# Optimization experiments

Hardware: AMD Instinct MI355X
Metric: run time of the kernel (lower is better)

## Reference

```python
import math
import jax, jax.numpy as jnp
import numpy as np

B, N, W, D, H = 16, 64, 128, 128, 4

def posenc(L, d):
    pos = jnp.arange(L, dtype=jnp.float32)[:, None]
    div = jnp.exp(jnp.arange(0, d, 2, dtype=jnp.float32) * (-math.log(10000.0) / d))
    pe = jnp.zeros((L, d), jnp.float32)
    pe = pe.at[:, 0::2].set(jnp.sin(pos * div))
    pe = pe.at[:, 1::2].set(jnp.cos(pos * div))
    return pe

def ln(x):
    # torch nn.LayerNorm(x.shape[1:]) created fresh each call: normalize over all non-batch dims, no affine
    ax = tuple(range(1, x.ndim))
    m = x.mean(ax, keepdims=True)
    v = ((x - m) ** 2).mean(ax, keepdims=True)
    return (x - m) / jnp.sqrt(v + 1e-5)

def conv1d(x, w, b):
    # x [B,C,L], w [Cout,Cin,K] (torch layout), VALID padding
    y = jax.lax.conv_general_dilated(x, w, (1,), 'VALID', dimension_numbers=('NCH', 'OIH', 'NCH'))
    return y + b[None, :, None]

def convt1d(x, w, b, stride, pad):
    # torch ConvTranspose1d, w [Cin,Cout,K]
    K = w.shape[2]
    w_ = jnp.flip(w, 2).transpose(1, 0, 2)  # [Cout,Cin,K]
    y = jax.lax.conv_general_dilated(x, w_, (1,), [(K - 1 - pad, K - 1 - pad)],
                                     lhs_dilation=(stride,), dimension_numbers=('NCH', 'OIH', 'NCH'))
    return y + b[None, :, None]

def mha(q, k, v, wi, bi, wo, bo):
    # torch nn.MultiheadAttention(batch_first=True), H heads
    d = q.shape[-1]
    qp = q @ wi[:d].T + bi[:d]
    kp = k @ wi[d:2 * d].T + bi[d:2 * d]
    vp = v @ wi[2 * d:].T + bi[2 * d:]
    def heads(t):
        b_, l_, _ = t.shape
        return t.reshape(b_, l_, H, d // H).transpose(0, 2, 1, 3)
    qh, kh, vh = heads(qp), heads(kp), heads(vp)
    s = jnp.einsum('bhqd,bhkd->bhqk', qh, kh) / jnp.sqrt(jnp.asarray(d // H, qh.dtype))
    o = jnp.einsum('bhqk,bhkd->bhqd', jax.nn.softmax(s, -1), vh)
    b_, l_ = q.shape[0], q.shape[1]
    return o.transpose(0, 2, 1, 3).reshape(b_, l_, d) @ wo.T + bo


def setup_inputs():
    key = jax.random.key(0)
    ks = iter(jax.random.split(key, 64))
    def w(shape, s=0.05):
        return jax.random.normal(next(ks), shape, jnp.float32) * s
    inp = {}
    inp['tokens'] = jax.random.randint(next(ks), (B, N, W), 0, 257, jnp.int32)
    inp['emb_table'] = w((257, D), 1.0)
    for nm in ['ce', 'ct', 'cg', 'ces', 'cts']:
        inp['w_' + nm] = w((D, D, 3))
        inp['b_' + nm] = w((D,))
    inp['mha_wi'] = w((3 * D, D)); inp['mha_bi'] = w((3 * D,))
    inp['mha_wo'] = w((D, D)); inp['mha_bo'] = w((D,))
    s = 1.0 / math.sqrt(D)
    inp['tgt1'] = jax.random.uniform(next(ks), (1, D), jnp.float32, -s, s)
    inp['tgt2'] = jax.random.uniform(next(ks), (1, D), jnp.float32, -s, s)
    for nm in ['mu', 'lv', 'di']:
        inp['w_' + nm] = w((D, D)); inp['b_' + nm] = w((D,))
    inp['eps'] = jax.random.normal(next(ks), (B, D), jnp.float32)
    inp['dk_w'] = w((32, 32)); inp['dk_b'] = w((32,))
    inp['dv_w'] = w((32, 32)); inp['dv_b'] = w((32,))
    inp['wt1'] = w((32, 64, 3)); inp['bt1'] = w((64,))
    inp['wt2'] = w((64, 128, 3)); inp['bt2'] = w((128,))
    for nm in ['sq', 'sk', 'sv']:
        inp[nm + '_w'] = w((128, 128)); inp[nm + '_b'] = w((128,))
    inp['wt3'] = w((128, 128, 3)); inp['bt3'] = w((128,))
    return inp


def reference(tokens, emb_table, w_ce, b_ce, w_ct, b_ct, w_cg, b_cg, w_ces, b_ces, w_cts, b_cts,
              mha_wi, mha_bi, mha_wo, mha_bo, tgt1, tgt2,
              w_mu, b_mu, w_lv, b_lv, w_di, b_di, eps,
              dk_w, dk_b, dv_w, dv_b, wt1, bt1, wt2, bt2,
              sq_w, sq_b, sk_w, sk_b, sv_w, sv_b, wt3, bt3):
    emb = emb_table[tokens] + posenc(W, D)                    # [B,N,W,D]
    flat = emb.reshape(B * N, W, D)                           # batch the per-sample torch loop

    def word_branch(wc, bc, act):
        h = act(conv1d(flat.transpose(0, 2, 1), wc, bc)).transpose(0, 2, 1)  # [BN,W-2,D]
        return mha(h, h, h, mha_wi, mha_bi, mha_wo, mha_bo)

    a_e = jax.nn.elu(word_branch(w_ce, b_ce, jax.nn.elu))
    a_t = jnp.tanh(word_branch(w_ct, b_ct, jnp.tanh))
    xw = ln((a_e * a_t).reshape(B, N, W - 2, D)).reshape(B * N, W - 2, D)

    h = jax.nn.elu(conv1d(xw.transpose(0, 2, 1), w_cg, b_cg)).transpose(0, 2, 1)  # [BN,W-4,D]
    q1 = jnp.broadcast_to(tgt1[None], (B * N, 1, D))
    out = mha(q1, h, h, mha_wi, mha_bi, mha_wo, mha_bo)[:, 0, :].reshape(B, N, D)

    se = out + posenc(N, D)                                   # sentence level

    def sent_branch(wc, bc, act):
        hh = act(conv1d(se.transpose(0, 2, 1), wc, bc)).transpose(0, 2, 1)       # [B,N-2,D]
        return mha(hh, hh, hh, mha_wi, mha_bi, mha_wo, mha_bo)

    s_e = jax.nn.elu(sent_branch(w_ces, b_ces, jax.nn.elu))
    s_t = jnp.tanh(sent_branch(w_cts, b_cts, jnp.tanh))
    xs = ln(s_e * s_t)
    q2 = jnp.broadcast_to(tgt2[None], (B, 1, D))
    doc = mha(q2, xs, xs, mha_wi, mha_bi, mha_wo, mha_bo)[:, 0, :]

    mu = doc @ w_mu.T + b_mu
    lv = doc @ w_lv.T + b_lv
    z = mu + eps * jnp.exp(0.5 * lv)

    h = (z @ w_di.T + b_di).reshape(B, 32, -1)                # [B,32,4]
    L = h.shape[2]
    k = jnp.einsum('oi,bil->bol', dk_w, h) + dk_b[None, :, None]
    v = jnp.einsum('oi,bil->bol', dv_w, h) + dv_b[None, :, None]
    kh = k.reshape(B, H, 8, L)
    vh = v.reshape(B, H, 8, L)
    att = jax.nn.softmax(jnp.einsum('bhdl,bhdm->bhlm', kh, vh) / jnp.sqrt(8.0), -1)
    h = jax.nn.elu(jnp.einsum('bhlm,bhdm->bhld', att, vh).reshape(B, 32, L))
    h = jax.nn.elu(ln(convt1d(h, wt1, bt1, 2, 1)))            # [B,64,7]
    h = jax.nn.elu(ln(convt1d(h, wt2, bt2, 2, 1)))            # [B,128,13]
    L2 = h.shape[2]
    qc = jnp.einsum('oi,bil->bol', sq_w, h) + sq_b[None, :, None]
    kc = jnp.einsum('oi,bil->bol', sk_w, h) + sk_b[None, :, None]
    vc = jnp.einsum('oi,bil->bol', sv_w, h) + sv_b[None, :, None]
    qh = qc.reshape(B, H, 32, L2)
    khh = kc.reshape(B, H, 32, L2)
    att = jax.nn.softmax(jnp.einsum('bhdl,bhdm->bhlm', qh, khh) / jnp.sqrt(32.0), -1)
    vr = vc.reshape(B, H, 32, L2).reshape(B, H, L2, 32)       # faithful torch .view reinterpretation
    h = jax.nn.elu(jnp.einsum('bhlm,bhmd->bhld', att, vr).reshape(B, 128, L2))
    recon = jax.nn.sigmoid(ln(convt1d(h, wt3, bt3, 1, 1)))    # [B,128,13]
    return recon, mu, lv
```

## Files before the change

### kernel.cpp

```cpp
#include <hip/hip_runtime.h>
#include <hip/hip_bf16.h>

typedef __hip_bfloat16 bf16;
typedef __attribute__((ext_vector_type(8))) short bf16x8;
typedef __attribute__((ext_vector_type(4))) float f32x4;

__device__ __forceinline__ float b2f(bf16 x){ return __bfloat162float(x); }
__device__ __forceinline__ bf16  f2b(float x){ return __float2bfloat16(x); }
__device__ __forceinline__ unsigned short b2u(bf16 x){ union{bf16 b; unsigned short u;} c; c.b = x; return c.u; }

#define LOG2E 1.4426950408889634f
#define QSC (0.17677669529663687f * LOG2E)

__device__ __forceinline__ float fexp2(float x){
  float r; asm("v_exp_f32 %0, %1" : "=v"(r) : "v"(x)); return r;
}
__device__ __forceinline__ float fast_exp(float x){ return fexp2(x * LOG2E); }
__device__ __forceinline__ float eluf(float x){ return x > 0.f ? x : fast_exp(x) - 1.f; }
__device__ __forceinline__ float fast_tanh(float x){
  float cx = fminf(fmaxf(x, -15.f), 15.f);
  float t = fexp2(cx * (2.f*LOG2E));
  return (t - 1.f) / (t + 1.f);
}

#define PE_C (-0.07195578415606394f)

__device__ __forceinline__ float pe_val(int pos, int d){
  int j2 = d & ~1;
  float ang = (float)pos * expf((float)j2 * PE_C);
  return (d & 1) ? cosf(ang) : sinf(ang);
}

__device__ __forceinline__ void pack_one(const float* __restrict__ W, bf16* __restrict__ out,
                                         int K, int N, int conv, int qscale, int t){
  int j = t & 7, lane = (t >> 3) & 63;
  int rest = t >> 9; int NT = N >> 4;
  int nt = rest % NT; int kb = rest / NT;
  int k = kb*32 + ((lane >> 4) << 3) + j;
  int n = nt*16 + (lane & 15);
  float v = conv ? W[n*384 + (k & 127)*3 + (k >> 7)] : W[(long)n*K + k];
  if (qscale && n < 128) v *= QSC;
  out[t] = f2b(v);
}

__global__ void k_prep(const float* __restrict__ w_ce, const float* __restrict__ w_ct,
                       const float* __restrict__ w_cg, const float* __restrict__ w_ces,
                       const float* __restrict__ w_cts, const float* __restrict__ wi,
                       const float* __restrict__ wo,
                       bf16* P_CE, bf16* P_CT, bf16* P_CG, bf16* P_CES, bf16* P_CTS,
                       bf16* P_WI, bf16* P_WO, float* __restrict__ pet){
  int bid = blockIdx.x;
  if (bid < 1152){
    int grp = bid / 192; int t = (bid % 192)*256 + threadIdx.x;
    const float* W; bf16* out; int K, N, conv, qs = 0;
    if      (grp == 0){ W = w_ce;  out = P_CE;  K=384; N=128; conv=1; }
    else if (grp == 1){ W = w_ct;  out = P_CT;  K=384; N=128; conv=1; }
    else if (grp == 2){ W = w_cg;  out = P_CG;  K=384; N=128; conv=1; }
    else if (grp == 3){ W = w_ces; out = P_CES; K=384; N=128; conv=1; }
    else if (grp == 4){ W = w_cts; out = P_CTS; K=384; N=128; conv=1; }
    else              { W = wi;    out = P_WI;  K=128; N=384; conv=0; qs=1; }
    pack_one(W, out, K, N, conv, qs, t);
  } else if (bid < 1216){
    int t = (bid - 1152)*256 + threadIdx.x;
    pack_one(wo, P_WO, 128, 128, 0, 0, t);
  } else {
    int i = (bid - 1216)*256 + threadIdx.x;
    if (i < 16384) pet[i] = pe_val(i >> 7, i & 127);
  }
}

__global__ void k_qprep(const float* __restrict__ wi, const float* __restrict__ bi,
                        const float* __restrict__ t1, const float* __restrict__ t2,
                        float* __restrict__ rkv){
  int tid = threadIdx.x;
  __shared__ float qps[256];
  {
    int which = tid >> 7, jj = tid & 127;
    const float* t = which ? t2 : t1;
    float a = bi[jj];
    for (int i = 0; i < 128; ++i) a += wi[jj*128 + i] * t[i];
    qps[tid] = a;
  }
  __syncthreads();
  int i = tid & 127, which = tid >> 7;
  for (int h = 0; h < 4; ++h){
    float a = 0.f;
    for (int d = 0; d < 32; ++d) a += qps[which*128 + h*32 + d] * wi[(128 + h*32 + d)*128 + i];
    rkv[which*512 + h*128 + i] = a;
  }
}

__global__ void k_embed8(const int* __restrict__ tok, const float* __restrict__ tab,
                         const float* __restrict__ pet, bf16* __restrict__ out){
  int t = blockIdx.x*256 + threadIdx.x;
  int q = t & 15;
  int flat = t >> 4; int w = flat & 127;
  int tk = tok[flat];
  const float* ta = tab + tk*128 + q*8;
  const float* pe = pet + (w << 7) + q*8;
  bf16 ob[8];
  #pragma unroll
  for (int i = 0; i < 8; ++i) ob[i] = f2b(ta[i] + pe[i]);
  *(f32x4*)(out + (size_t)t*8) = *(f32x4*)ob;
}

__global__ void k_se(const bf16* __restrict__ in, const float* __restrict__ pet, bf16* __restrict__ out){
  int idx = blockIdx.x*256 + threadIdx.x;
  int d = idx & 127; int n = (idx >> 7) & 63;
  out[idx] = f2b(b2f(in[idx]) + pet[(n << 7) + d]);
}

__global__ __launch_bounds__(256)
void k_gemm_mfma(const bf16* __restrict__ A, const bf16* __restrict__ Bp_, const bf16* __restrict__ Bp2,
                 const float* __restrict__ bias_, const float* __restrict__ bias2,
                 bf16* __restrict__ C_, bf16* __restrict__ C2p,
                 const bf16* __restrict__ mul,
                 int M, int K, int a_lout, int a_lind, int lda,
                 int NT, int n0t, int ldc, int act_, int act2,
                 const float* __restrict__ lnst, int lngrp){
  const bf16* Bp = Bp_; const float* bias = bias_; bf16* C = C_; int act = act_;
  if (blockIdx.z){ Bp = Bp2; bias = bias2; C = C2p; act = act2; }

  __shared__ f32x4 AsV[2][512];
  char* As0 = (char*)AsV[0];
  char* As1 = (char*)AsV[1];
  int tid = threadIdx.x;
  int lane = tid & 63, wave = tid >> 6;
  int wm = wave >> 1, wn = wave & 1;
  int m0 = blockIdx.x*128;
  int by = blockIdx.y;

  long offA[2]; bool okA[2]; float lnm[2], lnr[2]; int sbyte[2];
  #pragma unroll
  for (int p = 0; p < 2; ++p){
    int e = tid + p*256;
    int row = e >> 2, kq = e & 3, m = m0 + row;
    okA[p] = (m < M);
    long off = 0;
    if (okA[p]){
      off = (a_lout > 0) ? (long)(m / a_lout)*a_lind + (long)(m % a_lout)*128 + kq*8
                         : (long)m*lda + kq*8;
    }
    offA[p] = off;
    lnm[p] = 0.f; lnr[p] = 1.f;
    if (lnst && okA[p]){ int g = (int)(off / (long)lngrp); lnm[p] = lnst[2*g]; lnr[p] = lnst[2*g+1]; }
    sbyte[p] = (row*64 + kq*16) ^ ((row & 7) << 4);
  }
  auto loadA = [&](int p, int kb)->float4{
    float4 v = make_float4(0.f,0.f,0.f,0.f);
    if (okA[p]){
      v = *(const float4*)(A + offA[p] + kb*32);
      if (lnst){
        bf16* pp = (bf16*)&v; bf16 oo[8];
        #pragma unroll
        for (int u = 0; u < 8; ++u) oo[u] = f2b((b2f(pp[u]) - lnm[p]) * lnr[p]);
        v = *(float4*)&oo[0];
      }
    }
    return v;
  };

  const bf16* bptr[4];
  size_t bstep = (size_t)NT*512;
  #pragma unroll
  for (int fn = 0; fn < 4; ++fn){
    int ntile = n0t + by*8 + wn*4 + fn;
    bptr[fn] = Bp + ((size_t)ntile*64 + lane)*8;
  }
  int abyte[4];
  #pragma unroll
  for (int fm = 0; fm < 4; ++fm){
    int row = wm*64 + fm*16 + (lane & 15);
    abyte[fm] = (row*64 + ((lane >> 4) << 4)) ^ ((row & 7) << 4);
  }

  f32x4 acc[4][4];
  #pragma unroll
  for (int i = 0; i < 4; ++i)
    #pragma unroll
    for (int j = 0; j < 4; ++j) acc[i][j] = (f32x4){0.f,0.f,0.f,0.f};

  float4 va0 = loadA(0, 0), va1 = loadA(1, 0);
  *(float4*)(As0 + sbyte[0]) = va0;
  *(float4*)(As0 + sbyte[1]) = va1;
  __syncthreads();

  int nk = K >> 5;
  for (int kb = 0; kb < nk; ++kb){
    char* cur = (kb & 1) ? As1 : As0;
    char* nxt = (kb & 1) ? As0 : As1;
    bool more = (kb + 1) < nk;
    if (more){ va0 = loadA(0, kb+1); va1 = loadA(1, kb+1); }
    bf16x8 bfr[4];
    #pragma unroll
    for (int fn = 0; fn < 4; ++fn) bfr[fn] = *(const bf16x8*)(bptr[fn] + (size_t)kb*bstep);
    bf16x8 afr[4];
    #pragma unroll
    for (int fm = 0; fm < 4; ++fm) afr[fm] = *(const bf16x8*)(cur + abyte[fm]);
    #pragma unroll
    for (int fm = 0; fm < 4; ++fm)
      #pragma unroll
      for (int fn = 0; fn < 4; ++fn)
        acc[fm][fn] = __builtin_amdgcn_mfma_f32_16x16x32_bf16(afr[fm], bfr[fn], acc[fm][fn], 0, 0, 0);
    if (more){
      *(float4*)(nxt + sbyte[0]) = va0;
      *(float4*)(nxt + sbyte[1]) = va1;
    }
    __syncthreads();
  }

  #pragma unroll
  for (int fm = 0; fm < 4; ++fm){
    #pragma unroll
    for (int r = 0; r < 4; ++r){
      int m = m0 + wm*64 + fm*16 + ((lane >> 4) << 2) + r;
      if (m >= M) continue;
      #pragma unroll
      for (int fn = 0; fn < 4; ++fn){
        int n = by*128 + wn*64 + fn*16 + (lane & 15);
        float v = acc[fm][fn][r] + (bias ? bias[n] : 0.f);
        if (act == 1) v = eluf(v);
        else if (act == 2) v = fast_tanh(v);
        if (mul) v *= b2f(mul[(long)m*ldc + n]);
        C[(long)m*ldc + n] = f2b(v);
      }
    }
  }
}

template<int L>
__global__ __launch_bounds__(256)
void k_attn_fused(const bf16* __restrict__ X, const bf16* __restrict__ Pwi,
                  const float* __restrict__ bi, bf16* __restrict__ o){
  constexpr int KB  = (L + 31) / 32;
  constexpr int MT  = KB * 2;
  constexpr int WMT = MT / 4;
  constexpr int NP  = KB * 32;
  constexpr int PRS = NP * 2;

  __shared__ alignas(16) char As[NP*256];
  __shared__ alignas(16) char Qb[NP*64];
  __shared__ alignas(16) char Kb[NP*64];
  __shared__ alignas(16) char Vt[32*PRS];
  char* Pb = As;

  int tid = threadIdx.x;
  int s = blockIdx.x >> 2, h = blockIdx.x & 3;
  const bf16* xb = X + (size_t)s*L*128;

  for (int e = tid; e < NP*16; e += 256){
    int row = e >> 4, c = e & 15;
    float4 v = make_float4(0.f,0.f,0.f,0.f);
    if (row < L) v = *(const float4*)(xb + (size_t)row*128 + c*8);
    *(float4*)(As + ((row*256 + c*16) ^ ((row & 7) << 4))) = v;
  }
  __syncthreads();

  int lane = tid & 63, wave = tid >> 6;
  int col = lane & 15;

  __builtin_amdgcn_s_setprio(1);
  #pragma unroll
  for (int mt = 0; mt < WMT; ++mt){
    int mtile = wave*WMT + mt;
    int arow = mtile*16 + col;
    bf16x8 a4[4];
    #pragma unroll
    for (int kb = 0; kb < 4; ++kb)
      a4[kb] = *(const bf16x8*)(As + ((arow*256 + kb*64 + ((lane >> 4) << 4)) ^ ((arow & 7) << 4)));
    #pragma unroll
    for (int which = 0; which < 3; ++which){
      f32x4 av[2];
      #pragma unroll
      for (int nt = 0; nt < 2; ++nt){
        int ntile = which*8 + h*2 + nt;
        float bia = bi[which*128 + h*32 + nt*16 + col];
        if (which == 0) bia *= QSC;
        av[nt] = (f32x4){bia, bia, bia, bia};
        #pragma unroll
        for (int kb = 0; kb < 4; ++kb){
          bf16x8 bfr = *(const bf16x8*)(Pwi + (((size_t)kb*24 + ntile)*64 + lane)*8);
          av[nt] = __builtin_amdgcn_mfma_f32_16x16x32_bf16(a4[kb], bfr, av[nt], 0, 0, 0);
        }
      }
      #pragma unroll
      for (int r = 0; r < 4; ++r){
        int row = mtile*16 + ((lane >> 4) << 2) + r;
        if (which < 2){
          unsigned pk = (unsigned)b2u(f2b(av[0][r])) | ((unsigned)b2u(f2b(av[1][r])) << 16);
          char* dst = which ? Kb : Qb;
          *(unsigned*)(dst + ((row*64 + col*4) ^ ((row & 7) << 4))) = pk;
        } else {
          int pos = (row & 15)*MT + (row >> 4);
          #pragma unroll
          for (int nt = 0; nt < 2; ++nt){
            int d = nt*16 + col;
            *(bf16*)(Vt + ((d*PRS + pos*2) ^ ((d & 7) << 4))) = f2b(av[nt][r]);
          }
        }
      }
    }
  }
  __builtin_amdgcn_s_setprio(0);
  __syncthreads();

  f32x4 acc[WMT][MT];
  #pragma unroll
  for (int mt = 0; mt < WMT; ++mt)
    #pragma unroll
    for (int nt = 0; nt < MT; ++nt) acc[mt][nt] = (f32x4){0.f,0.f,0.f,0.f};

  bf16x8 af[WMT];
  #pragma unroll
  for (int mt = 0; mt < WMT; ++mt){
    int row = (wave*WMT + mt)*16 + col;
    af[mt] = *(const bf16x8*)(Qb + ((row*64 + ((lane >> 4) << 4)) ^ ((row & 7) << 4)));
  }
  __builtin_amdgcn_s_setprio(1);
  #pragma unroll
  for (int nt = 0; nt < MT; ++nt){
    int rk2 = nt*16 + col;
    bf16x8 bfk = *(const bf16x8*)(Kb + ((rk2*64 + ((lane >> 4) << 4)) ^ ((rk2 & 7) << 4)));
    #pragma unroll
    for (int mt = 0; mt < WMT; ++mt)
      acc[mt][nt] = __builtin_amdgcn_mfma_f32_16x16x32_bf16(af[mt], bfk, acc[mt][nt], 0, 0, 0);
  }
  __builtin_amdgcn_s_setprio(0);

  const bool lastMask = col >= (L - (MT-1)*16);
  float pinv[WMT][4];
  #pragma unroll
  for (int mt = 0; mt < WMT; ++mt){
    #pragma unroll
    for (int r = 0; r < 4; ++r){
      float mx = -1e30f;
      #pragma unroll
      for (int nt = 0; nt < MT; ++nt){
        float v = acc[mt][nt][r];
        if (nt == MT-1 && lastMask){ v = -1e30f; acc[mt][nt][r] = v; }
        mx = fmaxf(mx, v);
      }
      mx = fmaxf(mx, __shfl_xor(mx, 1));
      mx = fmaxf(mx, __shfl_xor(mx, 2));
      mx = fmaxf(mx, __shfl_xor(mx, 4));
      mx = fmaxf(mx, __shfl_xor(mx, 8));
      float sum = 0.f;
      bf16 prow[MT];
      #pragma unroll
      for (int nt = 0; nt < MT; ++nt){
        float p = fexp2(acc[mt][nt][r] - mx);
        prow[nt] = f2b(p);
        sum += p;
      }
      sum += __shfl_xor(sum, 1);
      sum += __shfl_xor(sum, 2);
      sum += __shfl_xor(sum, 4);
      sum += __shfl_xor(sum, 8);
      pinv[mt][r] = 1.f / sum;
      int row = (wave*WMT + mt)*16 + ((lane >> 4) << 2) + r;
      char* dst = Pb + ((row*PRS + col*(MT*2)) ^ ((row & 7) << 4));
      if constexpr (MT == 8) *(f32x4*)dst = *(f32x4*)prow;
      else                   *(float2*)dst = *(float2*)prow;
    }
  }

  #pragma unroll
  for (int mt = 0; mt < WMT; ++mt){
    int mtile = wave*WMT + mt;
    f32x4 o0 = (f32x4){0.f,0.f,0.f,0.f}, o1 = (f32x4){0.f,0.f,0.f,0.f};
    __builtin_amdgcn_s_setprio(1);
    #pragma unroll
    for (int kb = 0; kb < KB; ++kb){
      int row = mtile*16 + col;
      bf16x8 pa = *(const bf16x8*)(Pb + ((row*PRS + kb*64 + ((lane >> 4) << 4)) ^ ((row & 7) << 4)));
      int d0 = col;
      bf16x8 v0 = *(const bf16x8*)(Vt + ((d0*PRS + kb*64 + ((lane >> 4) << 4)) ^ ((d0 & 7) << 4)));
      bf16x8 v1 = *(const bf16x8*)(Vt + (((d0+16)*PRS + kb*64 + ((lane >> 4) << 4)) ^ (((d0+16) & 7) << 4)));
      o0 = __builtin_amdgcn_mfma_f32_16x16x32_bf16(pa, v0, o0, 0, 0, 0);
      o1 = __builtin_amdgcn_mfma_f32_16x16x32_bf16(pa, v1, o1, 0, 0, 0);
    }
    __builtin_amdgcn_s_setprio(0);
    #pragma unroll
    for (int r = 0; r < 4; ++r){
      int row = mtile*16 + ((lane >> 4) << 2) + r;
      if (row < L){
        size_t ob = ((size_t)s*L + row)*128 + h*32 + col;
        o[ob]      = f2b(o0[r] * pinv[mt][r]);
        o[ob + 16] = f2b(o1[r] * pinv[mt][r]);
      }
    }
  }
}

template<int L>
__global__ __launch_bounds__(256)
void k_attn_tgt(const bf16* __restrict__ hin, const float* __restrict__ rk,
                const float* __restrict__ wi, const float* __restrict__ bi,
                bf16* __restrict__ outp){
  __shared__ alignas(16) char Hs[L*256];
  __shared__ float RKs[512];
  __shared__ float Ps[512];
  __shared__ float Cs[512];
  int tid = threadIdx.x, lane = tid & 63, wave = tid >> 6;
  int s = blockIdx.x;
  const bf16* hb = hin + (size_t)s*L*128;
  for (int e = tid; e < L*16; e += 256){
    int row = e >> 4, c = e & 15;
    *(float4*)(Hs + row*256 + ((c ^ (row & 7)) << 4)) = *(const float4*)(hb + row*128 + c*8);
  }
  for (int e = tid; e < 512; e += 256) RKs[e] = rk[e];
  __syncthreads();

  int j0 = lane, j1 = lane + 64;
  float v0 = -1e30f, v1 = -1e30f;
  if (j0 < L){
    float a = 0.f;
    #pragma unroll
    for (int c = 0; c < 16; ++c){
      bf16x8 x = *(const bf16x8*)(Hs + j0*256 + ((c ^ (j0 & 7)) << 4));
      #pragma unroll
      for (int u = 0; u < 8; ++u) a += b2f(((bf16*)&x)[u]) * RKs[wave*128 + c*8 + u];
    }
    v0 = a * 0.17677669529663687f;
  }
  if (j1 < L){
    float a = 0.f;
    #pragma unroll
    for (int c = 0; c < 16; ++c){
      bf16x8 x = *(const bf16x8*)(Hs + j1*256 + ((c ^ (j1 & 7)) << 4));
      #pragma unroll
      for (int u = 0; u < 8; ++u) a += b2f(((bf16*)&x)[u]) * RKs[wave*128 + c*8 + u];
    }
    v1 = a * 0.17677669529663687f;
  }
  float mx = fmaxf(v0, v1);
  #pragma unroll
  for (int off = 32; off; off >>= 1) mx = fmaxf(mx, __shfl_xor(mx, off));
  float e0 = (j0 < L) ? fast_exp(v0 - mx) : 0.f;
  float e1 = (j1 < L) ? fast_exp(v1 - mx) : 0.f;
  float sum = e0 + e1;
  #pragma unroll
  for (int off = 32; off; off >>= 1) sum += __shfl_xor(sum, off);
  float inv = 1.f / sum;
  Ps[wave*128 + j0] = e0 * inv;
  Ps[wave*128 + j1] = e1 * inv;

  int i0 = lane*2;
  float c0 = 0.f, c1 = 0.f;
  for (int j = 0; j < L; ++j){
    float p = Ps[wave*128 + j];
    short2 w2 = *(const short2*)(Hs + j*256 + (((i0 >> 3) ^ (j & 7)) << 4) + (i0 & 7)*2);
    c0 += p * b2f(*(bf16*)&w2.x);
    c1 += p * b2f(*(bf16*)&w2.y);
  }
  Cs[wave*128 + i0]     = c0;
  Cs[wave*128 + i0 + 1] = c1;
  __syncthreads();

  if (tid < 128){
    int h2 = tid >> 5;
    float a = bi[256 + tid];
    const float* wr = wi + (size_t)(256 + tid)*128;
    for (int i = 0; i < 128; ++i) a += wr[i] * Cs[h2*128 + i];
    outp[(size_t)s*128 + tid] = f2b(a);
  }
}

__global__ void k_ln_partial(const bf16* __restrict__ x, float* __restrict__ part, int GS, int P){
  int pi = blockIdx.x % P;
  int chunk8 = GS / P / 8;
  size_t base = (size_t)(blockIdx.x / P)*GS + (size_t)pi*(GS/P);
  float s = 0.f, s2 = 0.f;
  for (int i = threadIdx.x; i < chunk8; i += 256){
    f32x4 raw = *(const f32x4*)(x + base + (size_t)i*8);
    const bf16* xb = (const bf16*)&raw;
    #pragma unroll
    for (int j = 0; j < 8; ++j){ float v = b2f(xb[j]); s += v; s2 += v*v; }
  }
  #pragma unroll
  for (int off = 32; off; off >>= 1){ s += __shfl_xor(s, off); s2 += __shfl_xor(s2, off); }
  __shared__ float sh[8];
  int lane = threadIdx.x & 63, wv = threadIdx.x >> 6;
  if (lane == 0){ sh[wv] = s; sh[4 + wv] = s2; }
  __syncthreads();
  if (threadIdx.x == 0){
    part[blockIdx.x*2]     = sh[0]+sh[1]+sh[2]+sh[3];
    part[blockIdx.x*2 + 1] = sh[4]+sh[5]+sh[6]+sh[7];
  }
}

__global__ void k_ln_fin(const float* __restrict__ part, float* __restrict__ stats, int P, int GS){
  int g = blockIdx.x;
  float s = 0.f, s2 = 0.f;
  for (int i = threadIdx.x; i < P; i += 256){ s += part[(g*P + i)*2]; s2 += part[(g*P + i)*2 + 1]; }
  #pragma unroll
  for (int off = 32; off; off >>= 1){ s += __shfl_xor(s, off); s2 += __shfl_xor(s2, off); }
  __shared__ float sh[8];
  int lane = threadIdx.x & 63, wv = threadIdx.x >> 6;
  if (lane == 0){ sh[wv] = s; sh[4 + wv] = s2; }
  __syncthreads();
  if (threadIdx.x == 0){
    float S = sh[0]+sh[1]+sh[2]+sh[3], S2 = sh[4]+sh[5]+sh[6]+sh[7];
    float mean = S / GS;
    float var = S2 / GS - mean*mean;
    stats[g*2] = mean; stats[g*2 + 1] = rsqrtf(var + 1e-5f);
  }
}

__global__ void k_ln_small_bf16(const bf16* __restrict__ x, bf16* __restrict__ y, int n){
  int g = blockIdx.x;
  const bf16* xb = x + (size_t)g*n;
  bf16* yb = y + (size_t)g*n;
  float s = 0.f, s2 = 0.f;
  for (int i = threadIdx.x; i < n; i += 256){ float v = b2f(xb[i]); s += v; s2 += v*v; }
  #pragma unroll
  for (int off = 32; off; off >>= 1){ s += __shfl_xor(s, off); s2 += __shfl_xor(s2, off); }
  __shared__ float sh[8];  __shared__ float ms[2];
  int lane = threadIdx.x & 63, wv = threadIdx.x >> 6;
  if (lane == 0){ sh[wv] = s; sh[4 + wv] = s2; }
  __syncthreads();
  if (threadIdx.x == 0){
    float S = sh[0]+sh[1]+sh[2]+sh[3], S2 = sh[4]+sh[5]+sh[6]+sh[7];
    float mean = S / n;
    ms[0] = mean; ms[1] = rsqrtf(S2 / n - mean*mean + 1e-5f);
  }
  __syncthreads();
  float mean = ms[0], inv = ms[1];
  for (int i = threadIdx.x; i < n; i += 256) yb[i] = f2b((b2f(xb[i]) - mean)*inv);
}

__global__ __launch_bounds__(256)
void k_decoder(const bf16* __restrict__ DOC,
               const float* __restrict__ w_mu, const float* __restrict__ b_mu,
               const float* __restrict__ w_lv, const float* __restrict__ b_lv,
               const float* __restrict__ eps,
               const float* __restrict__ w_di, const float* __restrict__ b_di,
               const float* __restrict__ dk_w, const float* __restrict__ dk_b,
               const float* __restrict__ dv_w, const float* __restrict__ dv_b,
               const float* __restrict__ wt1, const float* __restrict__ bt1,
               const float* __restrict__ wt2, const float* __restrict__ bt2,
               const float* __restrict__ sq_w, const float* __restrict__ sq_b,
               const float* __restrict__ sk_w, const float* __restrict__ sk_b,
               const float* __restrict__ sv_w, const float* __restrict__ sv_b,
               const float* __restrict__ wt3, const float* __restrict__ bt3,
               float* __restrict__ dout){
  int b = blockIdx.x, tid = threadIdx.x;
  __shared__ float Zs[128], H3[128], KD[128], VD[128], D1[128];
  __shared__ float C1[448], D2[448];
  __shared__ float C2a[1664], D3[1664];
  __shared__ float QC[1664], KC[1664], VC[1664], D4[1664], C3a[1664];
  __shared__ float sc[676];
  __shared__ float red[8], ms[2];

  auto lnact = [&](const float* x, float* y, int n, int act){
    float s = 0.f, s2 = 0.f;
    for (int i = tid; i < n; i += 256){ float v = x[i]; s += v; s2 += v*v; }
    #pragma unroll
    for (int o = 32; o; o >>= 1){ s += __shfl_xor(s, o); s2 += __shfl_xor(s2, o); }
    int lane = tid & 63, wv = tid >> 6;
    if (lane == 0){ red[wv] = s; red[4+wv] = s2; }
    __syncthreads();
    if (tid == 0){
      float S = red[0]+red[1]+red[2]+red[3], S2 = red[4]+red[5]+red[6]+red[7];
      float mean = S/n; ms[0] = mean; ms[1] = rsqrtf(S2/n - mean*mean + 1e-5f);
    }
    __syncthreads();
    float mean = ms[0], inv = ms[1];
    for (int i = tid; i < n; i += 256){
      float v = (x[i]-mean)*inv;
      if (act == 1) v = eluf(v);
      else if (act == 3) v = 1.f/(1.f + fast_exp(-v));
      y[i] = v;
    }
    __syncthreads();
  };

  if (tid < 128){
    const bf16* dr = DOC + b*128;
    float mu = b_mu[tid], lv = b_lv[tid];
    for (int i = 0; i < 128; ++i){
      float x = b2f(dr[i]);
      mu += x * w_mu[tid*128 + i];
      lv += x * w_lv[tid*128 + i];
    }
    dout[26624 + b*128 + tid] = mu;
    dout[28672 + b*128 + tid] = lv;
    Zs[tid] = mu + eps[b*128 + tid] * fast_exp(0.5f*lv);
  }
  __syncthreads();
  if (tid < 128){
    float a = b_di[tid];
    for (int i = 0; i < 128; ++i) a += Zs[i] * w_di[tid*128 + i];
    H3[tid] = a;
  }
  __syncthreads();
  if (tid < 128){
    int l = tid & 3, o2 = tid >> 2;
    float ak = dk_b[o2], av = dv_b[o2];
    for (int i = 0; i < 32; ++i){
      float xv = H3[i*4 + l];
      ak += dk_w[o2*32 + i]*xv;
      av += dv_w[o2*32 + i]*xv;
    }
    KD[tid] = ak; VD[tid] = av;
  }
  __syncthreads();
  if (tid < 64){
    int h = tid >> 4, l = (tid >> 2) & 3, m = tid & 3;
    float a = 0.f;
    #pragma unroll
    for (int d = 0; d < 8; ++d) a += KD[(h*8+d)*4 + l] * VD[(h*8+d)*4 + m];
    sc[tid] = a * 0.35355339059327373f;
  }
  __syncthreads();
  if (tid < 16){
    int base = tid*4;
    float mx = fmaxf(fmaxf(sc[base],sc[base+1]),fmaxf(sc[base+2],sc[base+3]));
    float e0=fast_exp(sc[base]-mx), e1=fast_exp(sc[base+1]-mx), e2=fast_exp(sc[base+2]-mx), e3=fast_exp(sc[base+3]-mx);
    float inv = 1.f/(e0+e1+e2+e3);
    sc[base]=e0*inv; sc[base+1]=e1*inv; sc[base+2]=e2*inv; sc[base+3]=e3*inv;
  }
  __syncthreads();
  if (tid < 128){
    int h = tid >> 5, rem = tid & 31, l = rem >> 3, d = rem & 7;
    float a = 0.f;
    #pragma unroll
    for (int m = 0; m < 4; ++m) a += sc[h*16 + l*4 + m] * VD[(h*8+d)*4 + m];
    D1[tid] = eluf(a);
  }
  __syncthreads();
  for (int idx = tid; idx < 448; idx += 256){
    int co = idx / 7, lo = idx % 7;
    float a = bt1[co];
    for (int k = 0; k < 3; ++k){
      int t = lo + 1 - k;
      if (t < 0 || (t & 1)) continue;
      int li = t >> 1; if (li >= 4) continue;
      float aa = 0.f;
      for (int ci = 0; ci < 32; ++ci) aa += D1[ci*4 + li] * wt1[ci*192 + co*3 + k];
      a += aa;
    }
    C1[idx] = a;
  }
  __syncthreads();
  lnact(C1, D2, 448, 1);
  for (int idx = tid; idx < 1664; idx += 256){
    int co = idx / 13, lo = idx % 13;
    float a = bt2[co];
    for (int k = 0; k < 3; ++k){
      int t = lo + 1 - k;
      if (t < 0 || (t & 1)) continue;
      int li = t >> 1; if (li >= 7) continue;
      float aa = 0.f;
      for (int ci = 0; ci < 64; ++ci) aa += D2[ci*7 + li] * wt2[ci*384 + co*3 + k];
      a += aa;
    }
    C2a[idx] = a;
  }
  __syncthreads();
  lnact(C2a, D3, 1664, 1);
  for (int idx = tid; idx < 1664; idx += 256){
    int o = idx / 13, l = idx % 13;
    float a1 = sq_b[o], a2 = sk_b[o], a3 = sv_b[o];
    for (int i = 0; i < 128; ++i){
      float xv = D3[i*13 + l];
      a1 += sq_w[o*128 + i]*xv;
      a2 += sk_w[o*128 + i]*xv;
      a3 += sv_w[o*128 + i]*xv;
    }
    QC[idx] = a1; KC[idx] = a2; VC[idx] = a3;
  }
  __syncthreads();
  for (int idx = tid; idx < 676; idx += 256){
    int h = idx / 169, rem = idx % 169;
    int l = rem / 13, m = rem % 13;
    float a = 0.f;
    #pragma unroll
    for (int d = 0; d < 32; ++d) a += QC[h*416 + d*13 + l] * KC[h*416 + d*13 + m];
    sc[idx] = a * 0.17677669529663687f;
  }
  __syncthreads();
  if (tid < 52){
    int h = tid / 13, l = tid % 13;
    float* row = sc + h*169 + l*13;
    float mx = -1e30f;
    for (int m = 0; m < 13; ++m) mx = fmaxf(mx, row[m]);
    float ssum = 0.f;
    for (int m = 0; m < 13; ++m){ float p = fast_exp(row[m]-mx); row[m] = p; ssum += p; }
    float inv = 1.f/ssum;
    for (int m = 0; m < 13; ++m) row[m] *= inv;
  }
  __syncthreads();
  for (int idx = tid; idx < 1664; idx += 256){
    int h = idx / 416, rem = idx % 416;
    int l = rem >> 5, d = rem & 31;
    float a = 0.f;
    for (int m = 0; m < 13; ++m) a += sc[h*169 + l*13 + m] * VC[h*416 + m*32 + d];
    D4[idx] = eluf(a);
  }
  __syncthreads();
  for (int idx = tid; idx < 1664; idx += 256){
    int co = idx / 13, lo = idx % 13;
    float a = bt3[co];
    for (int k = 0; k < 3; ++k){
      int li = lo + 1 - k;
      if (li < 0 || li >= 13) continue;
      float aa = 0.f;
      for (int ci = 0; ci < 128; ++ci) aa += D4[ci*13 + li] * wt3[ci*384 + co*3 + k];
      a += aa;
    }
    C3a[idx] = a;
  }
  __syncthreads();
  lnact(C3a, D4, 1664, 3);
  for (int i = tid; i < 1664; i += 256) dout[b*1664 + i] = D4[i];
}

extern "C" void kernel_launch(void* const* d_in, const int* in_sizes, int n_in,
                              void* d_out, int out_size, void* d_ws, size_t ws_size,
                              hipStream_t stream){
  const int*   tokens = (const int*)  d_in[0];
  const float* tab    = (const float*)d_in[1];
  const float* w_ce = (const float*)d_in[2];  const float* b_ce = (const float*)d_in[3];
  const float* w_ct = (const float*)d_in[4];  const float* b_ct = (const float*)d_in[5];
  const float* w_cg = (const float*)d_in[6];  const float* b_cg = (const float*)d_in[7];
  const float* w_ces= (const float*)d_in[8];  const float* b_ces= (const float*)d_in[9];
  const float* w_cts= (const float*)d_in[10]; const float* b_cts= (const float*)d_in[11];
  const float* wi   = (const float*)d_in[12]; const float* bi   = (const float*)d_in[13];
  const float* wo   = (const float*)d_in[14]; const float* bo   = (const float*)d_in[15];
  const float* tgt1 = (const float*)d_in[16]; const float* tgt2 = (const float*)d_in[17];
  const float* w_mu = (const float*)d_in[18]; const float* b_mu = (const float*)d_in[19];
  const float* w_lv = (const float*)d_in[20]; const float* b_lv = (const float*)d_in[21];
  const float* w_di = (const float*)d_in[22]; const float* b_di = (const float*)d_in[23];
  const float* epsb = (const float*)d_in[24];
  const float* dk_w = (const float*)d_in[25]; const float* dk_b = (const float*)d_in[26];
  const float* dv_w = (const float*)d_in[27]; const float* dv_b = (const float*)d_in[28];
  const float* wt1  = (const float*)d_in[29]; const float* bt1  = (const float*)d_in[30];
  const float* wt2  = (const float*)d_in[31]; const float* bt2  = (const float*)d_in[32];
  const float* sq_w = (const float*)d_in[33]; const float* sq_b = (const float*)d_in[34];
  const float* sk_w = (const float*)d_in[35]; const float* sk_b = (const float*)d_in[36];
  const float* sv_w = (const float*)d_in[37]; const float* sv_b = (const float*)d_in[38];
  const float* wt3  = (const float*)d_in[39]; const float* bt3  = (const float*)d_in[40];

  float* dout = (float*)d_out;

  char* ws = (char*)d_ws;
  size_t off = 0;
  auto take = [&](size_t bytes)->char*{ char* p = ws + off; off += (bytes + 255) & ~(size_t)255; return p; };
  bf16* EMB  = (bf16*)take(16777216ull*2);
  bf16* HB   = (bf16*)take(16515072ull*2);
  bf16* OB   = (bf16*)take(16515072ull*2);
  bf16* AE   = (bf16*)take(16515072ull*2);
  bf16* O1   = (bf16*)take(131072ull*2);
  bf16* OUTB = (bf16*)take(131072ull*2);
  bf16* SEB  = (bf16*)take(131072ull*2);
  bf16* SH   = (bf16*)take(126976ull*2);
  bf16* SCT  = (bf16*)take(126976ull*2);
  bf16* SO   = (bf16*)take(126976ull*2);
  bf16* SAE  = (bf16*)take(126976ull*2);
  bf16* XS   = (bf16*)take(126976ull*2);
  bf16* DO1  = (bf16*)take(2048ull*2);
  bf16* DOC  = (bf16*)take(2048ull*2);
  float* RK  = (float*)take(1024*4);
  float* PART= (float*)take(2016ull*2*4);
  float* STATS=(float*)take(32*4);
  float* PET = (float*)take(16384*4);
  bf16* P_CE = (bf16*)take(49152ull*2);
  bf16* P_CT = (bf16*)take(49152ull*2);
  bf16* P_CG = (bf16*)take(49152ull*2);
  bf16* P_CES= (bf16*)take(49152ull*2);
  bf16* P_CTS= (bf16*)take(49152ull*2);
  bf16* P_WI = (bf16*)take(49152ull*2);
  bf16* P_WO = (bf16*)take(16384ull*2);
  (void)ws_size; (void)in_sizes; (void)n_in; (void)out_size;

  auto cdiv = [](long a, long b){ return (int)((a + b - 1)/b); };
  auto gemm = [&](const bf16* A, const bf16* Bpp, const float* bias, bf16* C, const bf16* mul,
                  int M, int N, int K, int a_lout, int a_lind, int lda, int NT, int n0t, int ldc, int act,
                  const float* lnst, int lngrp){
    dim3 g(cdiv(M,128), N/128, 1);
    k_gemm_mfma<<<g, 256, 0, stream>>>(A, Bpp, Bpp, bias, bias, C, C, mul,
                                       M, K, a_lout, a_lind, lda, NT, n0t, ldc, act, act, lnst, lngrp);
  };
  auto gemmz = [&](const bf16* A, const bf16* Bp1, const float* b1, bf16* C1, int act1,
                   const bf16* Bp2, const float* b2, bf16* C2, int act2,
                   int M, int N, int K, int a_lout, int a_lind, int lda, int NT, int n0t, int ldc){
    dim3 g(cdiv(M,128), N/128, 2);
    k_gemm_mfma<<<g, 256, 0, stream>>>(A, Bp1, Bp2, b1, b2, C1, C2, nullptr,
                                       M, K, a_lout, a_lind, lda, NT, n0t, ldc, act1, act2, nullptr, 0);
  };

  k_prep<<<1280, 256, 0, stream>>>(w_ce, w_ct, w_cg, w_ces, w_cts, wi, wo,
                                   P_CE, P_CT, P_CG, P_CES, P_CTS, P_WI, P_WO, PET);
  k_qprep<<<1, 256, 0, stream>>>(wi, bi, tgt1, tgt2, RK);
  k_embed8<<<8192, 256, 0, stream>>>(tokens, tab, PET, EMB);

  gemmz(EMB, P_CE, b_ce, HB, 1, P_CT, b_ct, OB, 2, 129024, 128, 384, 126, 16384, 0, 8, 0, 128);

  k_attn_fused<126><<<4096, 256, 0, stream>>>(HB, P_WI, bi, EMB);
  gemm(EMB, P_WO, bo, AE, nullptr, 129024, 128, 128, 0, 0, 128, 8, 0, 128, 1, nullptr, 0);

  k_attn_fused<126><<<4096, 256, 0, stream>>>(OB, P_WI, bi, EMB);
  gemm(EMB, P_WO, bo, HB, AE, 129024, 128, 128, 0, 0, 128, 8, 0, 128, 2, nullptr, 0);

  k_ln_partial<<<2016, 256, 0, stream>>>(HB, PART, 1032192, 126);
  k_ln_fin<<<16, 256, 0, stream>>>(PART, STATS, 126, 1032192);

  gemm(HB, P_CG, b_cg, OB, nullptr, 126976, 128, 384, 124, 16128, 0, 8, 0, 128, 1, STATS, 1032192);

  k_attn_tgt<124><<<1024, 256, 0, stream>>>(OB, RK, wi, bi, O1);
  gemm(O1, P_WO, bo, OUTB, nullptr, 1024, 128, 128, 0, 0, 128, 8, 0, 128, 0, nullptr, 0);

  k_se<<<512, 256, 0, stream>>>(OUTB, PET, SEB);

  gemmz(SEB, P_CES, b_ces, SH, 1, P_CTS, b_cts, SCT, 2, 992, 128, 384, 62, 8192, 0, 8, 0, 128);

  k_attn_fused<62><<<64, 256, 0, stream>>>(SH, P_WI, bi, SO);
  gemm(SO, P_WO, bo, SAE, nullptr, 992, 128, 128, 0, 0, 128, 8, 0, 128, 1, nullptr, 0);

  k_attn_fused<62><<<64, 256, 0, stream>>>(SCT, P_WI, bi, SO);
  gemm(SO, P_WO, bo, SH, SAE, 992, 128, 128, 0, 0, 128, 8, 0, 128, 2, nullptr, 0);

  k_ln_small_bf16<<<16, 256, 0, stream>>>(SH, XS, 7936);

  k_attn_tgt<62><<<16, 256, 0, stream>>>(XS, RK + 512, wi, bi, DO1);
  gemm(DO1, P_WO, bo, DOC, nullptr, 16, 128, 128, 0, 0, 128, 8, 0, 128, 0, nullptr, 0);

  k_decoder<<<16, 256, 0, stream>>>(DOC, w_mu, b_mu, w_lv, b_lv, epsb, w_di, b_di,
                                    dk_w, dk_b, dv_w, dv_b, wt1, bt1, wt2, bt2,
                                    sq_w, sq_b, sk_w, sk_b, sv_w, sv_b, wt3, bt3, dout);
}
```

Before: 701.4 us.

## Split monolithic decoder kernel into multi-block stages for more parallelism

The single 16-block decoder kernel is broken into several launches: an initial stage, transposed convolutions spread over 128 blocks, a per-element channel projection, per-head attention over 64 blocks, and separate layernorm kernels. The goal is to spread the serial decoder tail across more CUs instead of 16. In exchange, intermediates now round-trip through global memory and there are extra kernel launches.

```diff
diff --git a/kernel.cpp b/kernel.cpp
--- a/kernel.cpp
+++ b/kernel.cpp
@@ -529,51 +529,48 @@
   for (int i = threadIdx.x; i < n; i += 256) yb[i] = f2b((b2f(xb[i]) - mean)*inv);
 }
 
+__global__ void k_ln_small_f32(const float* __restrict__ x, float* __restrict__ y, int n, int act){
+  int g = blockIdx.x;
+  const float* xb = x + (size_t)g*n;
+  float* yb = y + (size_t)g*n;
+  float s = 0.f, s2 = 0.f;
+  for (int i = threadIdx.x; i < n; i += 256){ float v = xb[i]; s += v; s2 += v*v; }
+  #pragma unroll
+  for (int off = 32; off; off >>= 1){ s += __shfl_xor(s, off); s2 += __shfl_xor(s2, off); }
+  __shared__ float sh[8];  __shared__ float ms[2];
+  int lane = threadIdx.x & 63, wv = threadIdx.x >> 6;
+  if (lane == 0){ sh[wv] = s; sh[4 + wv] = s2; }
+  __syncthreads();
+  if (threadIdx.x == 0){
+    float S = sh[0]+sh[1]+sh[2]+sh[3], S2 = sh[4]+sh[5]+sh[6]+sh[7];
+    float mean = S / n;
+    ms[0] = mean; ms[1] = rsqrtf(S2 / n - mean*mean + 1e-5f);
+  }
+  __syncthreads();
+  float mean = ms[0], inv = ms[1];
+  for (int i = threadIdx.x; i < n; i += 256){
+    float v = (xb[i] - mean)*inv;
+    if (act == 1) v = eluf(v);
+    else if (act == 3) v = 1.f/(1.f + fast_exp(-v));
+    yb[i] = v;
+  }
+}
+
 __global__ __launch_bounds__(256)
-void k_decoder(const bf16* __restrict__ DOC,
-               const float* __restrict__ w_mu, const float* __restrict__ b_mu,
-               const float* __restrict__ w_lv, const float* __restrict__ b_lv,
-               const float* __restrict__ eps,
-               const float* __restrict__ w_di, const float* __restrict__ b_di,
-               const float* __restrict__ dk_w, const float* __restrict__ dk_b,
-               const float* __restrict__ dv_w, const float* __restrict__ dv_b,
-               const float* __restrict__ wt1, const float* __restrict__ bt1,
-               const float* __restrict__ wt2, const float* __restrict__ bt2,
-               const float* __restrict__ sq_w, const float* __restrict__ sq_b,
-               const float* __restrict__ sk_w, const float* __restrict__ sk_b,
-               const float* __restrict__ sv_w, const float* __restrict__ sv_b,
-               const float* __restrict__ wt3, const float* __restrict__ bt3,
-               float* __restrict__ dout){
+void k_dec_a(const bf16* __restrict__ DOC,
+             const float* __restrict__ w_mu, const float* __restrict__ b_mu,
+             const float* __restrict__ w_lv, const float* __restrict__ b_lv,
+             const float* __restrict__ eps,
+             const float* __restrict__ w_di, const float* __restrict__ b_di,
+             const float* __restrict__ dk_w, const float* __restrict__ dk_b,
+             const float* __restrict__ dv_w, const float* __restrict__ dv_b,
+             const float* __restrict__ wt1, const float* __restrict__ bt1,
+             float* __restrict__ dout, float* __restrict__ DEC2){
   int b = blockIdx.x, tid = threadIdx.x;
   __shared__ float Zs[128], H3[128], KD[128], VD[128], D1[128];
-  __shared__ float C1[448], D2[448];
-  __shared__ float C2a[1664], D3[1664];
-  __shared__ float QC[1664], KC[1664], VC[1664], D4[1664], C3a[1664];
-  __shared__ float sc[676];
+  __shared__ float C1[448];
+  __shared__ float sc[64];
   __shared__ float red[8], ms[2];
-
-  auto lnact = [&](const float* x, float* y, int n, int act){
-    float s = 0.f, s2 = 0.f;
-    for (int i = tid; i < n; i += 256){ float v = x[i]; s += v; s2 += v*v; }
-    #pragma unroll
-    for (int o = 32; o; o >>= 1){ s += __shfl_xor(s, o); s2 += __shfl_xor(s2, o); }
-    int lane = tid & 63, wv = tid >> 6;
-    if (lane == 0){ red[wv] = s; red[4+wv] = s2; }
-    __syncthreads();
-    if (tid == 0){
-      float S = red[0]+red[1]+red[2]+red[3], S2 = red[4]+red[5]+red[6]+red[7];
-      float mean = S/n; ms[0] = mean; ms[1] = rsqrtf(S2/n - mean*mean + 1e-5f);
-    }
-    __syncthreads();
-    float mean = ms[0], inv = ms[1];
-    for (int i = tid; i < n; i += 256){
-      float v = (x[i]-mean)*inv;
-      if (act == 1) v = eluf(v);
-      else if (act == 3) v = 1.f/(1.f + fast_exp(-v));
-      y[i] = v;
-    }
-    __syncthreads();
-  };
 
   if (tid < 128){
     const bf16* dr = DOC + b*128;
@@ -643,77 +640,102 @@
     C1[idx] = a;
   }
   __syncthreads();
-  lnact(C1, D2, 448, 1);
-  for (int idx = tid; idx < 1664; idx += 256){
-    int co = idx / 13, lo = idx % 13;
-    float a = bt2[co];
-    for (int k = 0; k < 3; ++k){
-      int t = lo + 1 - k;
-      if (t < 0 || (t & 1)) continue;
-      int li = t >> 1; if (li >= 7) continue;
-      float aa = 0.f;
-      for (int ci = 0; ci < 64; ++ci) aa += D2[ci*7 + li] * wt2[ci*384 + co*3 + k];
-      a += aa;
-    }
-    C2a[idx] = a;
-  }
-  __syncthreads();
-  lnact(C2a, D3, 1664, 1);
-  for (int idx = tid; idx < 1664; idx += 256){
-    int o = idx / 13, l = idx % 13;
-    float a1 = sq_b[o], a2 = sk_b[o], a3 = sv_b[o];
-    for (int i = 0; i < 128; ++i){
-      float xv = D3[i*13 + l];
-      a1 += sq_w[o*128 + i]*xv;
-      a2 += sk_w[o*128 + i]*xv;
-      a3 += sv_w[o*128 + i]*xv;
-    }
-    QC[idx] = a1; KC[idx] = a2; VC[idx] = a3;
-  }
-  __syncthreads();
-  for (int idx = tid; idx < 676; idx += 256){
-    int h = idx / 169, rem = idx % 169;
-    int l = rem / 13, m = rem % 13;
+  {
+    float s = 0.f, s2 = 0.f;
+    for (int i = tid; i < 448; i += 256){ float v = C1[i]; s += v; s2 += v*v; }
+    #pragma unroll
+    for (int o = 32; o; o >>= 1){ s += __shfl_xor(s, o); s2 += __shfl_xor(s2, o); }
+    int lane = tid & 63, wv = tid >> 6;
+    if (lane == 0){ red[wv] = s; red[4+wv] = s2; }
+    __syncthreads();
+    if (tid == 0){
+      float S = red[0]+red[1]+red[2]+red[3], S2 = red[4]+red[5]+red[6]+red[7];
+      float mean = S/448.f; ms[0] = mean; ms[1] = rsqrtf(S2/448.f - mean*mean + 1e-5f);
+    }
+    __syncthreads();
+    float mean = ms[0], inv = ms[1];
+    for (int i = tid; i < 448; i += 256)
+      DEC2[b*448 + i] = eluf((C1[i]-mean)*inv);
+  }
+}
+
+__global__ void k_chanproj3(const float* __restrict__ x,
+                            const float* __restrict__ w1, const float* __restrict__ b1,
+                            const float* __restrict__ w2, const float* __restrict__ b2,
+                            const float* __restrict__ w3, const float* __restrict__ b3,
+                            float* __restrict__ y1, float* __restrict__ y2, float* __restrict__ y3,
+                            int Bn, int C, int L){
+  int idx = blockIdx.x*256 + threadIdx.x;
+  if (idx >= Bn*C*L) return;
+  int l = idx % L; int t2 = idx / L; int o = t2 % C; int b = t2 / C;
+  float a1 = b1[o], a2 = b2[o], a3 = b3[o];
+  const float* xb = x + (size_t)b*C*L + l;
+  for (int i = 0; i < C; ++i){
+    float xv = xb[i*L];
+    a1 += w1[(size_t)o*C + i]*xv;
+    a2 += w2[(size_t)o*C + i]*xv;
+    a3 += w3[(size_t)o*C + i]*xv;
+  }
+  y1[idx] = a1; y2[idx] = a2; y3[idx] = a3;
+}
+
+__global__ __launch_bounds__(256)
+void k_dec_attn2(const float* __restrict__ qc, const float* __restrict__ kc,
+                 const float* __restrict__ vc, float* __restrict__ out){
+  int b = blockIdx.x >> 2, h = blockIdx.x & 3, tid = threadIdx.x;
+  __shared__ float sc[169];
+  const float* qb = qc + b*1664 + h*416;
+  const float* kb = kc + b*1664 + h*416;
+  const float* vb = vc + b*1664 + h*416;
+  if (tid < 169){
+    int l = tid/13, m = tid - l*13;
     float a = 0.f;
     #pragma unroll
-    for (int d = 0; d < 32; ++d) a += QC[h*416 + d*13 + l] * KC[h*416 + d*13 + m];
-    sc[idx] = a * 0.17677669529663687f;
-  }
-  __syncthreads();
-  if (tid < 52){
-    int h = tid / 13, l = tid % 13;
-    float* row = sc + h*169 + l*13;
+    for (int d = 0; d < 32; ++d) a += qb[d*13 + l] * kb[d*13 + m];
+    sc[tid] = a * 0.17677669529663687f;
+  }
+  __syncthreads();
+  if (tid < 13){
     float mx = -1e30f;
-    for (int m = 0; m < 13; ++m) mx = fmaxf(mx, row[m]);
-    float ssum = 0.f;
-    for (int m = 0; m < 13; ++m){ float p = fast_exp(row[m]-mx); row[m] = p; ssum += p; }
-    float inv = 1.f/ssum;
-    for (int m = 0; m < 13; ++m) row[m] *= inv;
-  }
-  __syncthreads();
-  for (int idx = tid; idx < 1664; idx += 256){
-    int h = idx / 416, rem = idx % 416;
-    int l = rem >> 5, d = rem & 31;
+    for (int m = 0; m < 13; ++m) mx = fmaxf(mx, sc[tid*13 + m]);
+    float s = 0.f;
+    for (int m = 0; m < 13; ++m){ float p = fast_exp(sc[tid*13 + m] - mx); sc[tid*13 + m] = p; s += p; }
+    float inv = 1.f/s;
+    for (int m = 0; m < 13; ++m) sc[tid*13 + m] *= inv;
+  }
+  __syncthreads();
+  for (int idx = tid; idx < 416; idx += 256){
+    int l = idx >> 5, d = idx & 31;
     float a = 0.f;
-    for (int m = 0; m < 13; ++m) a += sc[h*169 + l*13 + m] * VC[h*416 + m*32 + d];
-    D4[idx] = eluf(a);
-  }
-  __syncthreads();
-  for (int idx = tid; idx < 1664; idx += 256){
-    int co = idx / 13, lo = idx % 13;
-    float a = bt3[co];
-    for (int k = 0; k < 3; ++k){
-      int li = lo + 1 - k;
-      if (li < 0 || li >= 13) continue;
-      float aa = 0.f;
-      for (int ci = 0; ci < 128; ++ci) aa += D4[ci*13 + li] * wt3[ci*384 + co*3 + k];
-      a += aa;
-    }
-    C3a[idx] = a;
-  }
-  __syncthreads();
-  lnact(C3a, D4, 1664, 3);
-  for (int i = tid; i < 1664; i += 256) dout[b*1664 + i] = D4[i];
+    for (int m = 0; m < 13; ++m) a += sc[l*13 + m] * vb[m*32 + d];
+    out[b*1664 + h*416 + idx] = eluf(a);
+  }
+}
+
+__global__ __launch_bounds__(256)
+void k_convt(const float* __restrict__ x, const float* __restrict__ w,
+             const float* __restrict__ bias, float* __restrict__ y,
+             int Bn, int Ci, int Co, int Lin, int Lout, int stride, int pad, int nch){
+  __shared__ float xs[1664];
+  int b = blockIdx.x / nch;
+  int c0 = (blockIdx.x % nch)*16;
+  int tid = threadIdx.x;
+  for (int i = tid; i < Ci*Lin; i += 256) xs[i] = x[(size_t)b*Ci*Lin + i];
+  __syncthreads();
+  int co = c0 + (tid & 15);
+  int lo = tid >> 4;
+  if (co >= Co || lo >= Lout) return;
+  float a = bias[co];
+  for (int k = 0; k < 3; ++k){
+    int t = lo + pad - k;
+    if (t < 0 || (t % stride)) continue;
+    int li = t / stride;
+    if (li >= Lin) continue;
+    float aa = 0.f;
+    for (int ci = 0; ci < Ci; ++ci) aa += xs[ci*Lin + li] * w[(size_t)ci*Co*3 + co*3 + k];
+    a += aa;
+  }
+  y[(size_t)b*Co*Lout + co*Lout + lo] = a;
 }
 
 extern "C" void kernel_launch(void* const* d_in, const int* in_sizes, int n_in,
@@ -764,6 +786,14 @@
   float* RK  = (float*)take(1024*4);
   float* PART= (float*)take(2016ull*2*4);
   float* STATS=(float*)take(32*4);
+  float* DEC2= (float*)take(7168*4);
+  float* C2  = (float*)take(26624*4);
+  float* DEC3= (float*)take(26624*4);
+  float* QC  = (float*)take(26624*4);
+  float* KC  = (float*)take(26624*4);
+  float* VC  = (float*)take(26624*4);
+  float* DEC4= (float*)take(26624*4);
+  float* C3  = (float*)take(26624*4);
   float* PET = (float*)take(16384*4);
   bf16* P_CE = (bf16*)take(49152ull*2);
   bf16* P_CT = (bf16*)take(49152ull*2);
@@ -783,10 +813,10 @@
                                        M, K, a_lout, a_lind, lda, NT, n0t, ldc, act, act, lnst, lngrp);
   };
   auto gemmz = [&](const bf16* A, const bf16* Bp1, const float* b1, bf16* C1, int act1,
-                   const bf16* Bp2, const float* b2, bf16* C2, int act2,
+                   const bf16* Bp2, const float* b2, bf16* C2p, int act2,
                    int M, int N, int K, int a_lout, int a_lind, int lda, int NT, int n0t, int ldc){
     dim3 g(cdiv(M,128), N/128, 2);
-    k_gemm_mfma<<<g, 256, 0, stream>>>(A, Bp1, Bp2, b1, b2, C1, C2, nullptr,
+    k_gemm_mfma<<<g, 256, 0, stream>>>(A, Bp1, Bp2, b1, b2, C1, C2p, nullptr,
                                        M, K, a_lout, a_lind, lda, NT, n0t, ldc, act1, act2, nullptr, 0);
   };
 
@@ -826,7 +856,13 @@
   k_attn_tgt<62><<<16, 256, 0, stream>>>(XS, RK + 512, wi, bi, DO1);
   gemm(DO1, P_WO, bo, DOC, nullptr, 16, 128, 128, 0, 0, 128, 8, 0, 128, 0, nullptr, 0);
 
-  k_decoder<<<16, 256, 0, stream>>>(DOC, w_mu, b_mu, w_lv, b_lv, epsb, w_di, b_di,
-                                    dk_w, dk_b, dv_w, dv_b, wt1, bt1, wt2, bt2,
-                                    sq_w, sq_b, sk_w, sk_b, sv_w, sv_b, wt3, bt3, dout);
-}
+  k_dec_a<<<16, 256, 0, stream>>>(DOC, w_mu, b_mu, w_lv, b_lv, epsb, w_di, b_di,
+                                  dk_w, dk_b, dv_w, dv_b, wt1, bt1, dout, DEC2);
+  k_convt<<<16*8, 256, 0, stream>>>(DEC2, wt2, bt2, C2, 16, 64, 128, 7, 13, 2, 1, 8);
+  k_ln_small_f32<<<16, 256, 0, stream>>>(C2, DEC3, 1664, 1);
+  k_chanproj3<<<cdiv(26624,256), 256, 0, stream>>>(DEC3, sq_w, sq_b, sk_w, sk_b, sv_w, sv_b,
+                                                   QC, KC, VC, 16, 128, 13);
+  k_dec_attn2<<<64, 256, 0, stream>>>(QC, KC, VC, DEC4);
+  k_convt<<<16*8, 256, 0, stream>>>(DEC4, wt3, bt3, C3, 16, 128, 128, 13, 13, 1, 1, 8);
+  k_ln_small_f32<<<16, 256, 0, stream>>>(C3, dout, 1664, 3);
+}
```

Measured after the change: 656.5 us. 1.07x faster.
